# Kernel optimization log

Measured on AMD Instinct MI355X. Metric: run time of the kernel, lower is better.

The kernel has to match this reference:

```python
import jax, jax.numpy as jnp
import numpy as np

B, T, D = 8, 8192, 768
H, HD = 12, 64            # heads, head_dim
Q_STRIDE = 4              # flattened 2x2 q pooling
WINDOW = 64               # flattened mask-unit size after pooling
SCALE = HD ** -0.5


def setup_inputs() -> dict:
    key = jax.random.key(0)
    ks = jax.random.split(key, 5)
    return {
        "embeddings": jax.random.normal(ks[0], (B, T, D), jnp.float32),
        "qkv_w": jax.random.normal(ks[1], (3 * D, D), jnp.float32) * 0.02,
        "qkv_b": jax.random.normal(ks[2], (3 * D,), jnp.float32) * 0.02,
        "proj_w": jax.random.normal(ks[3], (D, D), jnp.float32) * 0.02,
        "proj_b": jax.random.normal(ks[4], (D,), jnp.float32) * 0.02,
    }


def reference(embeddings, qkv_w, qkv_b, proj_w, proj_b):
    b, t, _ = embeddings.shape
    nw = t // (Q_STRIDE * WINDOW)          # number of mask-unit windows
    seq = t // nw                           # tokens per window (pre q-pool)
    # qkv: [b, t, 3D] -> [b, seq, nw, 3, H, HD] (windows are interleaved along tokens)
    qkv = (embeddings @ qkv_w.T + qkv_b).reshape(b, seq, nw, 3, H, HD)
    qkv = jnp.transpose(qkv, (3, 0, 4, 2, 1, 5))  # [3, b, H, nw, seq, HD]
    q, k, v = qkv[0], qkv[1], qkv[2]
    # q max-pool over stride groups (interleaved split of seq)
    q = q.reshape(b, H, nw, Q_STRIDE, seq // Q_STRIDE, HD).max(axis=3)
    attn = jax.nn.softmax(
        jnp.einsum("bhwqd,bhwkd->bhwqk", q * SCALE, k), axis=-1
    )  # [b, H, nw, q_len, seq]
    out = jnp.einsum("bhwqk,bhwkd->bhwqd", attn, v)  # [b, H, nw, q_len, HD]
    out = jnp.transpose(out, (0, 3, 2, 1, 4)).reshape(b, -1, H * HD)
    out = out @ proj_w.T + proj_b
    return out, attn
```

## Files before the change

kernel.cpp:

```cpp
#include <hip/hip_runtime.h>
#include <hip/hip_bf16.h>


typedef float  f32x4  __attribute__((ext_vector_type(4)));
typedef __bf16 bf16x8 __attribute__((ext_vector_type(8)));

__device__ __forceinline__ unsigned short f2bf(float f) {
  unsigned int u = __float_as_uint(f);
  u += 0x7fffu + ((u >> 16) & 1u);
  return (unsigned short)(u >> 16);
}
__device__ __forceinline__ float bf2f(unsigned short b) {
  return __uint_as_float(((unsigned int)b) << 16);
}

#define GLOAD_LDS16(gptr, lptr) __builtin_amdgcn_global_load_lds( \
    (const __attribute__((address_space(1))) void*)(gptr),        \
    (__attribute__((address_space(3))) void*)(lptr), 16, 0, 0)

__global__ void cvt_bf16(const float* __restrict__ src,
                         unsigned short* __restrict__ dst, int n4) {
  int i = blockIdx.x * blockDim.x + threadIdx.x;
  const int stride = gridDim.x * blockDim.x;
  for (; i < n4; i += stride) {
    const float4 v = ((const float4*)src)[i];
    ushort4 o;
    o.x = f2bf(v.x); o.y = f2bf(v.y); o.z = f2bf(v.z); o.w = f2bf(v.w);
    ((ushort4*)dst)[i] = o;
  }
}

template <int OUT_BF16>
__global__ __launch_bounds__(512, 2) void gemm256p(
    const unsigned short* __restrict__ A, const unsigned short* __restrict__ B,
    const float* __restrict__ bias, void* __restrict__ Cout,
    int M, int N, int K) {
  extern __shared__ char lds[];

  const int tid  = threadIdx.x;
  const int lane = tid & 63;
  const int wid  = tid >> 6;
  const int g16  = (lane >> 4) & 3;
  const int l15  = lane & 15;
  const int wm   = wid >> 2;
  const int wn   = wid & 3;

  const size_t bm = (size_t)blockIdx.x << 8;
  const int NT = K >> 6;
  const int NB = N >> 8;
  const int TT = NB * NT;

  const int srow = tid >> 2;
  const int csel = (((tid & 3) ^ ((tid >> 3) & 3)) << 3);
  const int ldst = wid * 1024;
  const unsigned short* pA0 = A + (bm + srow) * (size_t)K + csel;
  const unsigned short* pA1 = pA0 + (size_t)128 * K;
  const unsigned short* pB0 = B + (size_t)srow * K + csel;
  const unsigned short* pB1 = pB0 + (size_t)128 * K;

#define STAGE_A(koff, regbase)                                          \
  do {                                                                  \
    GLOAD_LDS16(pA0 + (koff), lds + (regbase) + ldst);                  \
    GLOAD_LDS16(pA1 + (koff), lds + (regbase) + 8192 + ldst);           \
  } while (0)
#define STAGE_B(boff, regbase)                                          \
  do {                                                                  \
    GLOAD_LDS16(pB0 + (boff), lds + (regbase) + ldst);                  \
    GLOAD_LDS16(pB1 + (boff), lds + (regbase) + 8192 + ldst);           \
  } while (0)

  const int s16  = ((g16 ^ ((l15 >> 1) & 3)) << 4);
  const int offA = (wm * 128 + l15) * 64 + s16;
  const int offB = (wn * 64 + l15) * 64 + s16;

  f32x4 acc[8][4];
  const f32x4 zero4 = {0.f, 0.f, 0.f, 0.f};
#pragma unroll
  for (int i = 0; i < 8; ++i)
#pragma unroll
    for (int j = 0; j < 4; ++j) acc[i][j] = zero4;

#define READ_A(par, kk, rh)                                              \
  { const char* rb = lds + (par) * 32768 + (kk) * 16384 + offA + (rh) * 4096; \
    af[0] = *(const bf16x8*)(rb);                                        \
    af[1] = *(const bf16x8*)(rb + 1024);                                 \
    af[2] = *(const bf16x8*)(rb + 2048);                                 \
    af[3] = *(const bf16x8*)(rb + 3072); }
#define READ_B(par, kk)                                                  \
  { const char* rb = lds + 65536 + (par) * 32768 + (kk) * 16384 + offB;  \
    bfv[0] = *(const bf16x8*)(rb);                                       \
    bfv[1] = *(const bf16x8*)(rb + 1024);                                \
    bfv[2] = *(const bf16x8*)(rb + 2048);                                \
    bfv[3] = *(const bf16x8*)(rb + 3072); }
#define MFMA16(rh)                                                       \
  _Pragma("unroll") for (int q = 0; q < 4; ++q)                          \
  _Pragma("unroll") for (int c = 0; c < 4; ++c)                          \
    acc[(rh) * 4 + q][c] = __builtin_amdgcn_mfma_f32_16x16x32_bf16(      \
        af[q], bfv[c], acc[(rh) * 4 + q][c], 0, 0, 0);
#define BAR() __builtin_amdgcn_s_barrier()
#define VMCNT8() asm volatile("s_waitcnt vmcnt(8)" ::: "memory")

  int    kk  = 0;
  int    bnC = 0;
  int    k1  = 64;
  int    k2  = 128;
  size_t rB1 = 0;
  size_t rB2 = 0;

  STAGE_A(0, 0);
  STAGE_B(0, 65536);
  STAGE_A(32, 16384);
  STAGE_B(32, 65536 + 16384);
  STAGE_A(64, 32768);
  STAGE_B(64, 65536 + 32768);
  VMCNT8();
  BAR();

  for (int s = 0; s < TT; ++s) {
    const int par  = s & 1;
    const int parn = par ^ 1;
    bf16x8 af[4], bfv[4];

    READ_A(par, 0, 0); READ_B(par, 0);
    STAGE_A(k1 + 32, parn * 32768 + 16384);
    BAR();
    __builtin_amdgcn_s_setprio(1); MFMA16(0); __builtin_amdgcn_s_setprio(0);
    BAR();

    READ_A(par, 0, 1);
    STAGE_B(rB1 + k1 + 32, 65536 + parn * 32768 + 16384);
    VMCNT8();
    BAR();
    __builtin_amdgcn_s_setprio(1); MFMA16(1); __builtin_amdgcn_s_setprio(0);
    BAR();

    READ_A(par, 1, 0); READ_B(par, 1);
    STAGE_A(k2, par * 32768);
    BAR();
    __builtin_amdgcn_s_setprio(1); MFMA16(0); __builtin_amdgcn_s_setprio(0);
    BAR();

    READ_A(par, 1, 1);
    STAGE_B(rB2 + k2, 65536 + par * 32768);
    VMCNT8();
    BAR();
    __builtin_amdgcn_s_setprio(1); MFMA16(1); __builtin_amdgcn_s_setprio(0);
    BAR();

    if (kk == NT - 1) {
#pragma unroll
      for (int ai = 0; ai < 8; ++ai) {
        const size_t row0 =
            bm + wm * 128 + (ai >> 2) * 64 + (ai & 3) * 16 + g16 * 4;
#pragma unroll
        for (int c = 0; c < 4; ++c) {
          const int col = bnC + wn * 64 + c * 16 + l15;
          const float bv = bias[col];
#pragma unroll
          for (int r = 0; r < 4; ++r) {
            const float v = acc[ai][c][r] + bv;
            const size_t idx = (row0 + r) * (size_t)N + col;
            if (OUT_BF16) ((unsigned short*)Cout)[idx] = f2bf(v);
            else          ((float*)Cout)[idx] = v;
          }
          acc[ai][c] = zero4;
        }
      }
      bnC += 256;
      kk = 0;
    } else {
      ++kk;
    }

    k1 = k2; rB1 = rB2;
    if (s + 3 < TT) {
      k2 += 64;
      if (k2 == K) { k2 = 0; rB2 += (size_t)256 * K; }
    }
  }
#undef STAGE_A
#undef STAGE_B
#undef READ_A
#undef READ_B
#undef MFMA16
#undef BAR
#undef VMCNT8
}

template <int OUT_BF16>
__global__ __launch_bounds__(256) void gemm_bt(
    const unsigned short* __restrict__ A, const unsigned short* __restrict__ B,
    const float* __restrict__ bias, void* __restrict__ Cout,
    int M, int N, int K) {
  __shared__ unsigned short As[128 * 64];
  __shared__ unsigned short Bs[128 * 64];

  const int tid  = threadIdx.x;
  const int lane = tid & 63;
  const int wid  = tid >> 6;
  const int g16  = lane >> 4;
  const int l15  = lane & 15;
  const int bm = blockIdx.x * 128;
  const int bn = blockIdx.y * 128;
  const int wr = (wid >> 1) * 64;
  const int wc = (wid & 1) * 64;

  const f32x4 zero4 = {0.f, 0.f, 0.f, 0.f};
  f32x4 acc[4][4];
#pragma unroll
  for (int m = 0; m < 4; ++m)
#pragma unroll
    for (int n = 0; n < 4; ++n) acc[m][n] = zero4;

  const int flatBase = tid * 16;
  const int rsw = l15 & 3;

  for (int kt = 0; kt < K; kt += 64) {
#pragma unroll
    for (int c = 0; c < 4; ++c) {
      const int flat = c * 4096 + flatBase;
      const int row  = flat >> 7;
      const int slot = (flat >> 4) & 7;
      const int cole = (((slot) ^ (row & 3)) << 3);
      const unsigned short* ga = A + (size_t)(bm + row) * K + kt + cole;
      const unsigned short* gb = B + (size_t)(bn + row) * K + kt + cole;
      GLOAD_LDS16(ga, (char*)As + c * 4096 + wid * 1024 + lane * 16);
      GLOAD_LDS16(gb, (char*)Bs + c * 4096 + wid * 1024 + lane * 16);
    }
    __syncthreads();
#pragma unroll
    for (int kk = 0; kk < 2; ++kk) {
      bf16x8 af[4], bfv[4];
#pragma unroll
      for (int m = 0; m < 4; ++m)
        af[m] = *(const bf16x8*)((const char*)As +
                 (wr + m * 16 + l15) * 128 + (((kk * 4 + g16) ^ rsw) << 4));
#pragma unroll
      for (int n = 0; n < 4; ++n)
        bfv[n] = *(const bf16x8*)((const char*)Bs +
                 (wc + n * 16 + l15) * 128 + (((kk * 4 + g16) ^ rsw) << 4));
#pragma unroll
      for (int m = 0; m < 4; ++m)
#pragma unroll
        for (int n = 0; n < 4; ++n)
          acc[m][n] = __builtin_amdgcn_mfma_f32_16x16x32_bf16(af[m], bfv[n],
                                                              acc[m][n], 0, 0, 0);
    }
    __syncthreads();
  }

#pragma unroll
  for (int n = 0; n < 4; ++n) {
    const int col = bn + wc + n * 16 + l15;
    const float bv = bias[col];
#pragma unroll
    for (int m = 0; m < 4; ++m) {
      const int rowb = bm + wr + m * 16 + g16 * 4;
#pragma unroll
      for (int r = 0; r < 4; ++r) {
        const float v = acc[m][n][r] + bv;
        const size_t idx = (size_t)(rowb + r) * N + col;
        if (OUT_BF16) ((unsigned short*)Cout)[idx] = f2bf(v);
        else          ((float*)Cout)[idx] = v;
      }
    }
  }
}

__global__ __launch_bounds__(256) void attn_kernel(
    const unsigned short* __restrict__ qkv,
    float* __restrict__ attn_out,
    unsigned short* __restrict__ Xws) {
  __shared__ unsigned short smem[32768];
  char* KP = (char*)smem;
  char* VT = (char*)(smem + 16384);

  const int tid  = threadIdx.x;
  const int lane = tid & 63;
  const int wid  = tid >> 6;
  const int g16  = lane >> 4;
  const int l15  = lane & 15;

  const int bid = blockIdx.x;
  const int w = bid & 31;
  const int h = (bid >> 5) % 12;
  const int b = bid / 384;

  const int s0 = tid >> 3;
  const int part = tid & 7;

#pragma unroll
  for (int p = 0; p < 8; ++p) {
    const int s = s0 + p * 32;
    const size_t gbase =
        ((size_t)b * 8192 + (size_t)s * 32 + w) * 2304 + h * 64 + part * 8;
    int4 kv = *(const int4*)(qkv + gbase + 768);
    *(int4*)(KP + ((s * 128 + part * 16) ^ ((s & 7) << 4))) = kv;
  }

#pragma unroll
  for (int p = 0; p < 2; ++p) {
    const int s = s0 * 4 + p * 128;
    const size_t gb0 =
        ((size_t)b * 8192 + (size_t)s * 32 + w) * 2304 + 1536 + h * 64 + part * 8;
    int4 x0 = *(const int4*)(qkv + gb0);
    int4 x1 = *(const int4*)(qkv + gb0 + 73728);
    int4 x2 = *(const int4*)(qkv + gb0 + 147456);
    int4 x3 = *(const int4*)(qkv + gb0 + 221184);
    const unsigned int* u0 = (const unsigned int*)&x0;
    const unsigned int* u1 = (const unsigned int*)&x1;
    const unsigned int* u2 = (const unsigned int*)&x2;
    const unsigned int* u3 = (const unsigned int*)&x3;
#pragma unroll
    for (int k = 0; k < 4; ++k) {
      const unsigned int lo01 = (u0[k] & 0xffffu) | (u1[k] << 16);
      const unsigned int lo23 = (u2[k] & 0xffffu) | (u3[k] << 16);
      const unsigned int hi01 = (u0[k] >> 16) | (u1[k] & 0xffff0000u);
      const unsigned int hi23 = (u2[k] >> 16) | (u3[k] & 0xffff0000u);
      const int dlo = part * 8 + 2 * k;
      const int dhi = dlo + 1;
      uint2 vlo; vlo.x = lo01; vlo.y = lo23;
      uint2 vhi; vhi.x = hi01; vhi.y = hi23;
      *(uint2*)(VT + ((dlo * 512 + s * 2) ^ ((dlo & 7) << 4))) = vlo;
      *(uint2*)(VT + ((dhi * 512 + s * 2) ^ ((dhi & 7) << 4))) = vhi;
    }
  }

  union BU { unsigned short u[8]; bf16x8 v; };
  BU aq0, aq1;
  {
    const int qrow = wid * 16 + l15;
    float q0[8], q1[8];
#pragma unroll
    for (int j = 0; j < 8; ++j) { q0[j] = -1e30f; q1[j] = -1e30f; }
#pragma unroll
    for (int g = 0; g < 4; ++g) {
      const size_t gbase =
          ((size_t)b * 8192 + (size_t)(g * 64 + qrow) * 32 + w) * 2304 +
          h * 64 + g16 * 8;
      int4 a = *(const int4*)(qkv + gbase);
      int4 c = *(const int4*)(qkv + gbase + 32);
      const unsigned short* pa = (const unsigned short*)&a;
      const unsigned short* pc = (const unsigned short*)&c;
#pragma unroll
      for (int j = 0; j < 8; ++j) {
        q0[j] = fmaxf(q0[j], bf2f(pa[j]));
        q1[j] = fmaxf(q1[j], bf2f(pc[j]));
      }
    }
#pragma unroll
    for (int j = 0; j < 8; ++j) {
      aq0.u[j] = (unsigned short)(__float_as_uint(q0[j]) >> 16);
      aq1.u[j] = (unsigned short)(__float_as_uint(q1[j]) >> 16);
    }
  }

  __syncthreads();

  f32x4 sacc[16];
  const f32x4 zero4 = {0.f, 0.f, 0.f, 0.f};
#pragma unroll
  for (int t = 0; t < 16; ++t) sacc[t] = zero4;
#pragma unroll
  for (int t = 0; t < 16; ++t) {
    const int srow = t * 16 + l15;
    bf16x8 bk0 = *(const bf16x8*)(KP + ((srow * 128 + 0  + g16 * 16) ^ ((srow & 7) << 4)));
    bf16x8 bk1 = *(const bf16x8*)(KP + ((srow * 128 + 64 + g16 * 16) ^ ((srow & 7) << 4)));
    sacc[t] = __builtin_amdgcn_mfma_f32_16x16x32_bf16(aq0.v, bk0, sacc[t], 0, 0, 0);
    sacc[t] = __builtin_amdgcn_mfma_f32_16x16x32_bf16(aq1.v, bk1, sacc[t], 0, 0, 0);
  }

  float inv_[4];
#pragma unroll
  for (int r = 0; r < 4; ++r) {
    float m = -1e30f;
#pragma unroll
    for (int t = 0; t < 16; ++t) { sacc[t][r] *= 0.125f; m = fmaxf(m, sacc[t][r]); }
#pragma unroll
    for (int off = 1; off < 16; off <<= 1) m = fmaxf(m, __shfl_xor(m, off, 64));
    float ssum = 0.f;
#pragma unroll
    for (int t = 0; t < 16; ++t) {
      float e = expf(sacc[t][r] - m);
      sacc[t][r] = e;
      ssum += e;
    }
#pragma unroll
    for (int off = 1; off < 16; off <<= 1) ssum += __shfl_xor(ssum, off, 64);
    inv_[r] = 1.f / ssum;
  }

  {
    float* ab = attn_out + ((size_t)bid * 64 + wid * 16) * 256;
#pragma unroll
    for (int t = 0; t < 16; ++t)
#pragma unroll
      for (int r = 0; r < 4; ++r) {
        const float p = sacc[t][r] * inv_[r];
        sacc[t][r] = p;
        ab[(size_t)(g16 * 4 + r) * 256 + t * 16 + l15] = p;
      }
  }

  __syncthreads();

  {
    char* PW = KP + wid * 8192;
#pragma unroll
    for (int t = 0; t < 16; ++t)
#pragma unroll
      for (int r = 0; r < 4; ++r) {
        const int row = g16 * 4 + r;
        *(unsigned short*)(PW + ((row * 512 + (t * 16 + l15) * 2) ^ ((row & 7) << 4))) =
            f2bf(sacc[t][r]);
      }
  }

  f32x4 oacc[4];
#pragma unroll
  for (int n = 0; n < 4; ++n) oacc[n] = zero4;
  {
    const char* PR = KP + wid * 8192;
#pragma unroll
    for (int kc = 0; kc < 8; ++kc) {
      bf16x8 pa = *(const bf16x8*)(PR + ((l15 * 512 + kc * 64 + g16 * 16) ^ ((l15 & 7) << 4)));
#pragma unroll
      for (int n = 0; n < 4; ++n) {
        const int d = n * 16 + l15;
        bf16x8 vv = *(const bf16x8*)(VT + ((d * 512 + kc * 64 + g16 * 16) ^ ((d & 7) << 4)));
        oacc[n] = __builtin_amdgcn_mfma_f32_16x16x32_bf16(pa, vv, oacc[n], 0, 0, 0);
      }
    }
  }

#pragma unroll
  for (int n = 0; n < 4; ++n)
#pragma unroll
    for (int r = 0; r < 4; ++r) {
      const int qi = wid * 16 + g16 * 4 + r;
      Xws[((size_t)b * 2048 + qi * 32 + w) * 768 + h * 64 + n * 16 + l15] =
          f2bf(oacc[n][r]);
    }
}

extern "C" void kernel_launch(void* const* d_in, const int* in_sizes, int n_in,
                              void* d_out, int out_size, void* d_ws, size_t ws_size,
                              hipStream_t stream) {
  const float* emb    = (const float*)d_in[0];
  const float* qkv_w  = (const float*)d_in[1];
  const float* qkv_b  = (const float*)d_in[2];
  const float* proj_w = (const float*)d_in[3];
  const float* proj_b = (const float*)d_in[4];
  float* out = (float*)d_out;

  char* ws = (char*)d_ws;
  unsigned short* embB   = (unsigned short*)(ws);
  unsigned short* wqkvB  = (unsigned short*)(ws + 100663296);
  unsigned short* wprojB = (unsigned short*)(ws + 104202240);
  unsigned short* qkvB   = (unsigned short*)(ws + 105381888);
  unsigned short* Xws    = (unsigned short*)(ws + 407371776);

  cvt_bf16<<<4096, 256, 0, stream>>>(emb, embB, 50331648 / 4);
  cvt_bf16<<<1728, 256, 0, stream>>>(qkv_w, wqkvB, 1769472 / 4);
  cvt_bf16<<<576, 256, 0, stream>>>(proj_w, wprojB, 589824 / 4);

  hipFuncSetAttribute(reinterpret_cast<const void*>(&gemm256p<1>),
                      hipFuncAttributeMaxDynamicSharedMemorySize, 131072);
  gemm256p<1><<<256, 512, 131072, stream>>>(embB, wqkvB, qkv_b, qkvB,
                                            65536, 2304, 768);

  attn_kernel<<<3072, 256, 0, stream>>>(qkvB, out + 12582912, Xws);

  gemm_bt<0><<<dim3(128, 6), 256, 0, stream>>>(Xws, wprojB, proj_b, out,
                                               16384, 768, 768);
}
```

Measured before the change: 482.4 us.

## Fuse fp32-to-bf16 activation conversion into QKV GEMM A-tile staging

Drops the separate kernel that converts the embeddings to bf16. The QKV GEMM now reads fp32 activations directly, packs them to bf16 in registers and writes them to LDS, which removes a full write and re-read of a large intermediate. The GEMM also changes from persistent blocks that loop over N tiles to one 256x256 tile per block across 2304 blocks, with a swizzled block-to-tile mapping. A-tile loads become synchronous register loads plus LDS stores instead of async global-to-LDS copies, which may expose load latency and double the A read bandwidth per tile.

```diff
diff --git a/kernel.cpp b/kernel.cpp
--- a/kernel.cpp
+++ b/kernel.cpp
@@ -31,8 +31,8 @@
 }
 
 template <int OUT_BF16>
-__global__ __launch_bounds__(512, 2) void gemm256p(
-    const unsigned short* __restrict__ A, const unsigned short* __restrict__ B,
+__global__ __launch_bounds__(512, 2) void gemm256f(
+    const float* __restrict__ A, const unsigned short* __restrict__ B,
     const float* __restrict__ bias, void* __restrict__ Cout,
     int M, int N, int K) {
   extern __shared__ char lds[];
@@ -45,23 +45,39 @@
   const int wm   = wid >> 2;
   const int wn   = wid & 3;
 
-  const size_t bm = (size_t)blockIdx.x << 8;
+  const int nbn = N >> 8;
+  const int wg  = (blockIdx.x & 7) * ((int)gridDim.x >> 3) + (blockIdx.x >> 3);
+  const size_t bm = (size_t)(wg / nbn) << 8;
+  const size_t bn = (size_t)(wg % nbn) << 8;
+
   const int NT = K >> 6;
-  const int NB = N >> 8;
-  const int TT = NB * NT;
 
   const int srow = tid >> 2;
   const int csel = (((tid & 3) ^ ((tid >> 3) & 3)) << 3);
+  const int dstb = tid * 16;
   const int ldst = wid * 1024;
-  const unsigned short* pA0 = A + (bm + srow) * (size_t)K + csel;
-  const unsigned short* pA1 = pA0 + (size_t)128 * K;
-  const unsigned short* pB0 = B + (size_t)srow * K + csel;
+  const float* pA0f = A + (bm + srow) * (size_t)K + csel;
+  const float* pA1f = pA0f + (size_t)128 * K;
+  const unsigned short* pB0 = B + (bn + srow) * (size_t)K + csel;
   const unsigned short* pB1 = pB0 + (size_t)128 * K;
 
-#define STAGE_A(koff, regbase)                                          \
-  do {                                                                  \
-    GLOAD_LDS16(pA0 + (koff), lds + (regbase) + ldst);                  \
-    GLOAD_LDS16(pA1 + (koff), lds + (regbase) + 8192 + ldst);           \
+#define STAGE_A(koff, regbase)                                           \
+  do {                                                                   \
+    const float4 x0 = *(const float4*)(pA0f + (koff));                   \
+    const float4 x1 = *(const float4*)(pA0f + (koff) + 4);               \
+    const float4 x2 = *(const float4*)(pA1f + (koff));                   \
+    const float4 x3 = *(const float4*)(pA1f + (koff) + 4);               \
+    int4 q0, q1;                                                         \
+    asm("v_cvt_pk_bf16_f32 %0, %1, %2" : "=v"(q0.x) : "v"(x0.x), "v"(x0.y)); \
+    asm("v_cvt_pk_bf16_f32 %0, %1, %2" : "=v"(q0.y) : "v"(x0.z), "v"(x0.w)); \
+    asm("v_cvt_pk_bf16_f32 %0, %1, %2" : "=v"(q0.z) : "v"(x1.x), "v"(x1.y)); \
+    asm("v_cvt_pk_bf16_f32 %0, %1, %2" : "=v"(q0.w) : "v"(x1.z), "v"(x1.w)); \
+    asm("v_cvt_pk_bf16_f32 %0, %1, %2" : "=v"(q1.x) : "v"(x2.x), "v"(x2.y)); \
+    asm("v_cvt_pk_bf16_f32 %0, %1, %2" : "=v"(q1.y) : "v"(x2.z), "v"(x2.w)); \
+    asm("v_cvt_pk_bf16_f32 %0, %1, %2" : "=v"(q1.z) : "v"(x3.x), "v"(x3.y)); \
+    asm("v_cvt_pk_bf16_f32 %0, %1, %2" : "=v"(q1.w) : "v"(x3.z), "v"(x3.w)); \
+    *(int4*)(lds + (regbase) + dstb)        = q0;                        \
+    *(int4*)(lds + (regbase) + 8192 + dstb) = q1;                        \
   } while (0)
 #define STAGE_B(boff, regbase)                                          \
   do {                                                                  \
@@ -98,14 +114,7 @@
     acc[(rh) * 4 + q][c] = __builtin_amdgcn_mfma_f32_16x16x32_bf16(      \
         af[q], bfv[c], acc[(rh) * 4 + q][c], 0, 0, 0);
 #define BAR() __builtin_amdgcn_s_barrier()
-#define VMCNT8() asm volatile("s_waitcnt vmcnt(8)" ::: "memory")
-
-  int    kk  = 0;
-  int    bnC = 0;
-  int    k1  = 64;
-  int    k2  = 128;
-  size_t rB1 = 0;
-  size_t rB2 = 0;
+#define LGKM0() asm volatile("s_waitcnt lgkmcnt(0)" ::: "memory")
 
   STAGE_A(0, 0);
   STAGE_B(0, 65536);
@@ -113,69 +122,57 @@
   STAGE_B(32, 65536 + 16384);
   STAGE_A(64, 32768);
   STAGE_B(64, 65536 + 32768);
-  VMCNT8();
+  LGKM0();
   BAR();
 
-  for (int s = 0; s < TT; ++s) {
-    const int par  = s & 1;
+  for (int t = 0; t < NT; ++t) {
+    const int par  = t & 1;
     const int parn = par ^ 1;
+    const int kc1  = (t + 1 < NT ? t + 1 : NT - 1) * 64;
+    const int kc2  = (t + 2 < NT ? t + 2 : NT - 1) * 64;
     bf16x8 af[4], bfv[4];
 
     READ_A(par, 0, 0); READ_B(par, 0);
-    STAGE_A(k1 + 32, parn * 32768 + 16384);
+    STAGE_A(kc1 + 32, parn * 32768 + 16384);
+    LGKM0();
     BAR();
     __builtin_amdgcn_s_setprio(1); MFMA16(0); __builtin_amdgcn_s_setprio(0);
     BAR();
 
     READ_A(par, 0, 1);
-    STAGE_B(rB1 + k1 + 32, 65536 + parn * 32768 + 16384);
-    VMCNT8();
+    STAGE_B(kc1 + 32, 65536 + parn * 32768 + 16384);
     BAR();
     __builtin_amdgcn_s_setprio(1); MFMA16(1); __builtin_amdgcn_s_setprio(0);
     BAR();
 
     READ_A(par, 1, 0); READ_B(par, 1);
-    STAGE_A(k2, par * 32768);
+    STAGE_A(kc2, par * 32768);
+    LGKM0();
     BAR();
     __builtin_amdgcn_s_setprio(1); MFMA16(0); __builtin_amdgcn_s_setprio(0);
     BAR();
 
     READ_A(par, 1, 1);
-    STAGE_B(rB2 + k2, 65536 + par * 32768);
-    VMCNT8();
+    STAGE_B(kc2, 65536 + par * 32768);
     BAR();
     __builtin_amdgcn_s_setprio(1); MFMA16(1); __builtin_amdgcn_s_setprio(0);
     BAR();
-
-    if (kk == NT - 1) {
-#pragma unroll
-      for (int ai = 0; ai < 8; ++ai) {
-        const size_t row0 =
-            bm + wm * 128 + (ai >> 2) * 64 + (ai & 3) * 16 + g16 * 4;
-#pragma unroll
-        for (int c = 0; c < 4; ++c) {
-          const int col = bnC + wn * 64 + c * 16 + l15;
-          const float bv = bias[col];
-#pragma unroll
-          for (int r = 0; r < 4; ++r) {
-            const float v = acc[ai][c][r] + bv;
-            const size_t idx = (row0 + r) * (size_t)N + col;
-            if (OUT_BF16) ((unsigned short*)Cout)[idx] = f2bf(v);
-            else          ((float*)Cout)[idx] = v;
-          }
-          acc[ai][c] = zero4;
-        }
-      }
-      bnC += 256;
-      kk = 0;
-    } else {
-      ++kk;
-    }
-
-    k1 = k2; rB1 = rB2;
-    if (s + 3 < TT) {
-      k2 += 64;
-      if (k2 == K) { k2 = 0; rB2 += (size_t)256 * K; }
+  }
+
+#pragma unroll
+  for (int ai = 0; ai < 8; ++ai) {
+    const size_t row0 = bm + wm * 128 + (ai >> 2) * 64 + (ai & 3) * 16 + g16 * 4;
+#pragma unroll
+    for (int c = 0; c < 4; ++c) {
+      const size_t col = bn + wn * 64 + c * 16 + l15;
+      const float bv = bias[col];
+#pragma unroll
+      for (int r = 0; r < 4; ++r) {
+        const float v = acc[ai][c][r] + bv;
+        const size_t idx = (row0 + r) * N + col;
+        if (OUT_BF16) ((unsigned short*)Cout)[idx] = f2bf(v);
+        else          ((float*)Cout)[idx] = v;
+      }
     }
   }
 #undef STAGE_A
@@ -184,7 +181,7 @@
 #undef READ_B
 #undef MFMA16
 #undef BAR
-#undef VMCNT8
+#undef LGKM0
 }
 
 template <int OUT_BF16>
@@ -454,20 +451,18 @@
   float* out = (float*)d_out;
 
   char* ws = (char*)d_ws;
-  unsigned short* embB   = (unsigned short*)(ws);
   unsigned short* wqkvB  = (unsigned short*)(ws + 100663296);
   unsigned short* wprojB = (unsigned short*)(ws + 104202240);
   unsigned short* qkvB   = (unsigned short*)(ws + 105381888);
   unsigned short* Xws    = (unsigned short*)(ws + 407371776);
 
-  cvt_bf16<<<4096, 256, 0, stream>>>(emb, embB, 50331648 / 4);
   cvt_bf16<<<1728, 256, 0, stream>>>(qkv_w, wqkvB, 1769472 / 4);
   cvt_bf16<<<576, 256, 0, stream>>>(proj_w, wprojB, 589824 / 4);
 
-  hipFuncSetAttribute(reinterpret_cast<const void*>(&gemm256p<1>),
+  hipFuncSetAttribute(reinterpret_cast<const void*>(&gemm256f<1>),
                       hipFuncAttributeMaxDynamicSharedMemorySize, 131072);
-  gemm256p<1><<<256, 512, 131072, stream>>>(embB, wqkvB, qkv_b, qkvB,
-                                            65536, 2304, 768);
+  gemm256f<1><<<2304, 512, 131072, stream>>>(emb, wqkvB, qkv_b, qkvB,
+                                             65536, 2304, 768);
 
   attn_kernel<<<3072, 256, 0, stream>>>(qkvB, out + 12582912, Xws);
 
```

New measurement: 591.5 us. +22.6%, slower.

## Replace projection GEMM with pipelined 256x256 tile kernel and merge weight conversions

Applied to the files above, without the earlier changes.

The output projection GEMM moves from a simple 128x128 tile kernel, which synchronizes after every K step, to a 256x256 tile kernel with 512 threads. The new kernel double-buffers LDS staging, keeps loads in flight with vmcnt waits, raises MFMA priority and swizzles the block order. The two weight fp32-to-bf16 conversion launches are also merged into one. The aim is to overlap global loads with MFMA work and cut a launch, but with M=16384 and N=768 only 192 blocks launch, which may leave part of the GPU idle.

```diff
diff --git a/kernel.cpp b/kernel.cpp
--- a/kernel.cpp
+++ b/kernel.cpp
@@ -27,6 +27,23 @@
     ushort4 o;
     o.x = f2bf(v.x); o.y = f2bf(v.y); o.z = f2bf(v.z); o.w = f2bf(v.w);
     ((ushort4*)dst)[i] = o;
+  }
+}
+
+__global__ void cvt_w2(const float* __restrict__ s1, unsigned short* __restrict__ d1,
+                       int n1_4,
+                       const float* __restrict__ s2, unsigned short* __restrict__ d2,
+                       int n2_4) {
+  int i = blockIdx.x * blockDim.x + threadIdx.x;
+  const int stride = gridDim.x * blockDim.x;
+  const int tot = n1_4 + n2_4;
+  for (; i < tot; i += stride) {
+    const float4 v = (i < n1_4) ? ((const float4*)s1)[i]
+                                : ((const float4*)s2)[i - n1_4];
+    ushort4 o;
+    o.x = f2bf(v.x); o.y = f2bf(v.y); o.z = f2bf(v.z); o.w = f2bf(v.w);
+    if (i < n1_4) ((ushort4*)d1)[i] = o;
+    else          ((ushort4*)d2)[i - n1_4] = o;
   }
 }
 
@@ -188,83 +205,140 @@
 }
 
 template <int OUT_BF16>
-__global__ __launch_bounds__(256) void gemm_bt(
+__global__ __launch_bounds__(512, 2) void gemm256t(
     const unsigned short* __restrict__ A, const unsigned short* __restrict__ B,
     const float* __restrict__ bias, void* __restrict__ Cout,
     int M, int N, int K) {
-  __shared__ unsigned short As[128 * 64];
-  __shared__ unsigned short Bs[128 * 64];
+  extern __shared__ char lds[];
 
   const int tid  = threadIdx.x;
   const int lane = tid & 63;
   const int wid  = tid >> 6;
-  const int g16  = lane >> 4;
+  const int g16  = (lane >> 4) & 3;
   const int l15  = lane & 15;
-  const int bm = blockIdx.x * 128;
-  const int bn = blockIdx.y * 128;
-  const int wr = (wid >> 1) * 64;
-  const int wc = (wid & 1) * 64;
-
+  const int wm   = wid >> 2;
+  const int wn   = wid & 3;
+
+  const int nbn = N >> 8;
+  const int wg  = (blockIdx.x & 7) * ((int)gridDim.x >> 3) + (blockIdx.x >> 3);
+  const size_t bm = (size_t)(wg / nbn) << 8;
+  const size_t bn = (size_t)(wg % nbn) << 8;
+
+  const int NT = K >> 6;
+
+  const int srow = tid >> 2;
+  const int csel = (((tid & 3) ^ ((tid >> 3) & 3)) << 3);
+  const int ldst = wid * 1024;
+  const unsigned short* pA0 = A + (bm + srow) * (size_t)K + csel;
+  const unsigned short* pA1 = pA0 + (size_t)128 * K;
+  const unsigned short* pB0 = B + (bn + srow) * (size_t)K + csel;
+  const unsigned short* pB1 = pB0 + (size_t)128 * K;
+
+#define STAGE(p0, p1, kcol, regbase)                                   \
+  do {                                                                 \
+    GLOAD_LDS16((p0) + (kcol), lds + (regbase) + ldst);                \
+    GLOAD_LDS16((p1) + (kcol), lds + (regbase) + 8192 + ldst);         \
+  } while (0)
+
+  const int s16  = ((g16 ^ ((l15 >> 1) & 3)) << 4);
+  const int offA = (wm * 128 + l15) * 64 + s16;
+  const int offB = (wn * 64 + l15) * 64 + s16;
+
+  f32x4 acc[8][4];
   const f32x4 zero4 = {0.f, 0.f, 0.f, 0.f};
-  f32x4 acc[4][4];
-#pragma unroll
-  for (int m = 0; m < 4; ++m)
-#pragma unroll
-    for (int n = 0; n < 4; ++n) acc[m][n] = zero4;
-
-  const int flatBase = tid * 16;
-  const int rsw = l15 & 3;
-
-  for (int kt = 0; kt < K; kt += 64) {
+#pragma unroll
+  for (int i = 0; i < 8; ++i)
+#pragma unroll
+    for (int j = 0; j < 4; ++j) acc[i][j] = zero4;
+
+#define READ_A(par, kk, rh)                                              \
+  { const char* rb = lds + (par) * 32768 + (kk) * 16384 + offA + (rh) * 4096; \
+    af[0] = *(const bf16x8*)(rb);                                        \
+    af[1] = *(const bf16x8*)(rb + 1024);                                 \
+    af[2] = *(const bf16x8*)(rb + 2048);                                 \
+    af[3] = *(const bf16x8*)(rb + 3072); }
+#define READ_B(par, kk)                                                  \
+  { const char* rb = lds + 65536 + (par) * 32768 + (kk) * 16384 + offB;  \
+    bfv[0] = *(const bf16x8*)(rb);                                       \
+    bfv[1] = *(const bf16x8*)(rb + 1024);                                \
+    bfv[2] = *(const bf16x8*)(rb + 2048);                                \
+    bfv[3] = *(const bf16x8*)(rb + 3072); }
+#define MFMA16(rh)                                                       \
+  _Pragma("unroll") for (int q = 0; q < 4; ++q)                          \
+  _Pragma("unroll") for (int c = 0; c < 4; ++c)                          \
+    acc[(rh) * 4 + q][c] = __builtin_amdgcn_mfma_f32_16x16x32_bf16(      \
+        af[q], bfv[c], acc[(rh) * 4 + q][c], 0, 0, 0);
+#define BAR() __builtin_amdgcn_s_barrier()
+#define VMCNT8() asm volatile("s_waitcnt vmcnt(8)" ::: "memory")
+
+  STAGE(pA0, pA1, 0, 0);
+  STAGE(pB0, pB1, 0, 65536);
+  STAGE(pA0, pA1, 32, 16384);
+  STAGE(pB0, pB1, 32, 65536 + 16384);
+  {
+    const int k1 = (NT > 1 ? 64 : 0);
+    STAGE(pA0, pA1, k1, 32768);
+    STAGE(pB0, pB1, k1, 65536 + 32768);
+  }
+  VMCNT8();
+  BAR();
+
+  for (int t = 0; t < NT; ++t) {
+    const int par  = t & 1;
+    const int parn = par ^ 1;
+    const int kc1  = (t + 1 < NT ? t + 1 : NT - 1) * 64;
+    const int kc2  = (t + 2 < NT ? t + 2 : NT - 1) * 64;
+    bf16x8 af[4], bfv[4];
+
+    READ_A(par, 0, 0); READ_B(par, 0);
+    STAGE(pA0, pA1, kc1 + 32, parn * 32768 + 16384);
+    BAR();
+    __builtin_amdgcn_s_setprio(1); MFMA16(0); __builtin_amdgcn_s_setprio(0);
+    BAR();
+
+    READ_A(par, 0, 1);
+    STAGE(pB0, pB1, kc1 + 32, 65536 + parn * 32768 + 16384);
+    VMCNT8();
+    BAR();
+    __builtin_amdgcn_s_setprio(1); MFMA16(1); __builtin_amdgcn_s_setprio(0);
+    BAR();
+
+    READ_A(par, 1, 0); READ_B(par, 1);
+    STAGE(pA0, pA1, kc2, par * 32768);
+    BAR();
+    __builtin_amdgcn_s_setprio(1); MFMA16(0); __builtin_amdgcn_s_setprio(0);
+    BAR();
+
+    READ_A(par, 1, 1);
+    STAGE(pB0, pB1, kc2, 65536 + par * 32768);
+    VMCNT8();
+    BAR();
+    __builtin_amdgcn_s_setprio(1); MFMA16(1); __builtin_amdgcn_s_setprio(0);
+    BAR();
+  }
+
+#pragma unroll
+  for (int ai = 0; ai < 8; ++ai) {
+    const size_t row0 = bm + wm * 128 + (ai >> 2) * 64 + (ai & 3) * 16 + g16 * 4;
 #pragma unroll
     for (int c = 0; c < 4; ++c) {
-      const int flat = c * 4096 + flatBase;
-      const int row  = flat >> 7;
-      const int slot = (flat >> 4) & 7;
-      const int cole = (((slot) ^ (row & 3)) << 3);
-      const unsigned short* ga = A + (size_t)(bm + row) * K + kt + cole;
-      const unsigned short* gb = B + (size_t)(bn + row) * K + kt + cole;
-      GLOAD_LDS16(ga, (char*)As + c * 4096 + wid * 1024 + lane * 16);
-      GLOAD_LDS16(gb, (char*)Bs + c * 4096 + wid * 1024 + lane * 16);
-    }
-    __syncthreads();
-#pragma unroll
-    for (int kk = 0; kk < 2; ++kk) {
-      bf16x8 af[4], bfv[4];
-#pragma unroll
-      for (int m = 0; m < 4; ++m)
-        af[m] = *(const bf16x8*)((const char*)As +
-                 (wr + m * 16 + l15) * 128 + (((kk * 4 + g16) ^ rsw) << 4));
-#pragma unroll
-      for (int n = 0; n < 4; ++n)
-        bfv[n] = *(const bf16x8*)((const char*)Bs +
-                 (wc + n * 16 + l15) * 128 + (((kk * 4 + g16) ^ rsw) << 4));
-#pragma unroll
-      for (int m = 0; m < 4; ++m)
-#pragma unroll
-        for (int n = 0; n < 4; ++n)
-          acc[m][n] = __builtin_amdgcn_mfma_f32_16x16x32_bf16(af[m], bfv[n],
-                                                              acc[m][n], 0, 0, 0);
-    }
-    __syncthreads();
-  }
-
-#pragma unroll
-  for (int n = 0; n < 4; ++n) {
-    const int col = bn + wc + n * 16 + l15;
-    const float bv = bias[col];
-#pragma unroll
-    for (int m = 0; m < 4; ++m) {
-      const int rowb = bm + wr + m * 16 + g16 * 4;
+      const size_t col = bn + wn * 64 + c * 16 + l15;
+      const float bv = bias[col];
 #pragma unroll
       for (int r = 0; r < 4; ++r) {
-        const float v = acc[m][n][r] + bv;
-        const size_t idx = (size_t)(rowb + r) * N + col;
+        const float v = acc[ai][c][r] + bv;
+        const size_t idx = (row0 + r) * N + col;
         if (OUT_BF16) ((unsigned short*)Cout)[idx] = f2bf(v);
         else          ((float*)Cout)[idx] = v;
       }
     }
   }
+#undef STAGE
+#undef READ_A
+#undef READ_B
+#undef MFMA16
+#undef BAR
+#undef VMCNT8
 }
 
 __global__ __launch_bounds__(256) void attn_kernel(
@@ -461,8 +535,8 @@
   unsigned short* Xws    = (unsigned short*)(ws + 407371776);
 
   cvt_bf16<<<4096, 256, 0, stream>>>(emb, embB, 50331648 / 4);
-  cvt_bf16<<<1728, 256, 0, stream>>>(qkv_w, wqkvB, 1769472 / 4);
-  cvt_bf16<<<576, 256, 0, stream>>>(proj_w, wprojB, 589824 / 4);
+  cvt_w2<<<2048, 256, 0, stream>>>(qkv_w, wqkvB, 1769472 / 4,
+                                   proj_w, wprojB, 589824 / 4);
 
   hipFuncSetAttribute(reinterpret_cast<const void*>(&gemm256p<1>),
                       hipFuncAttributeMaxDynamicSharedMemorySize, 131072);
@@ -471,6 +545,8 @@
 
   attn_kernel<<<3072, 256, 0, stream>>>(qkvB, out + 12582912, Xws);
 
-  gemm_bt<0><<<dim3(128, 6), 256, 0, stream>>>(Xws, wprojB, proj_b, out,
-                                               16384, 768, 768);
-}
+  hipFuncSetAttribute(reinterpret_cast<const void*>(&gemm256t<0>),
+                      hipFuncAttributeMaxDynamicSharedMemorySize, 131072);
+  gemm256t<0><<<192, 512, 131072, stream>>>(Xws, wprojB, proj_b, out,
+                                            16384, 768, 768);
+}
```

Result: faster. 464.7 us (median of 2 runs) (-3.7%).
